# Optimization experiments

Measured on AMD Instinct MI355X. Metric: run time of the kernel, lower is better.

Reference implementation:

```python
import jax, jax.numpy as jnp
import numpy as np

N_HEADS = 16
EPS = 1e-6

def _feature_map(x):
    return jax.nn.elu(x) + 1.0

def setup_inputs() -> dict:
    key = jax.random.key(0)
    k1, k2, k3 = jax.random.split(key, 3)
    B, S, D = 1, 2048, 1024
    x = jax.random.normal(k1, (B, S, D), dtype=jnp.float32)
    causal_mask = jnp.tril(jnp.ones((S, S), dtype=bool))[None, None]  # (1,1,S,S)
    # scale weights like nn.Linear default init (roughly 1/sqrt(fan_in))
    W_qkv = jax.random.normal(k2, (D, 3 * D), dtype=jnp.float32) / np.sqrt(D)
    W_out = jax.random.normal(k3, (D, D), dtype=jnp.float32) / np.sqrt(D)
    return {"x": x, "causal_mask": causal_mask, "W_qkv": W_qkv, "W_out": W_out}

def reference(x, causal_mask, W_qkv, W_out):
    B, S, D = x.shape
    H = N_HEADS
    hd = D // H
    qkv = x @ W_qkv                              # (B,S,3D)
    q, k, v = jnp.split(qkv, 3, axis=-1)
    def to_heads(t):
        return t.reshape(B, S, H, hd).transpose(0, 2, 1, 3)  # (B,H,S,hd)
    q, k, v = to_heads(q), to_heads(k), to_heads(v)
    phi_q = _feature_map(q)
    phi_k = _feature_map(k)
    k_cum = jnp.cumsum(phi_k, axis=2)                        # (B,H,S,hd)
    kv = jnp.einsum('bhsi,bhsj->bhsij', phi_k, v)            # (B,H,S,hd,hd)
    kv_cum = jnp.cumsum(kv, axis=2)
    numer = jnp.einsum('bhsi,bhsij->bhsj', phi_q, kv_cum)    # (B,H,S,hd)
    denom = jnp.einsum('bhsi,bhsi->bhs', phi_q, k_cum) + EPS
    attn_out = numer / denom[..., None]
    attn_out = attn_out.transpose(0, 2, 1, 3).reshape(B, S, D)
    return attn_out @ W_out
```

## Files before the change

### kernel.cpp

```cpp
#include <hip/hip_runtime.h>
#include <cstddef>
#include <cstdint>

#define SEQ 2048
#define DIM 1024
#define NH 16
#define HD 64
#define CK 64
#define NCK (SEQ / CK)
#define KVR 65
#define KVRP 80

typedef __attribute__((ext_vector_type(8))) short short8;
typedef __attribute__((ext_vector_type(8))) unsigned short ushort8;
typedef __attribute__((ext_vector_type(4))) float fx4;

__device__ __forceinline__ float phi_fn(float x) {
    return x > 0.f ? x + 1.f : __expf(x);
}
__device__ __forceinline__ float bf2f(unsigned short u) {
    return __uint_as_float((unsigned int)u << 16);
}
__device__ __forceinline__ unsigned short f2bf(float f) {
    unsigned int u = __float_as_uint(f);
    unsigned int r = (u + 0x7FFFu + ((u >> 16) & 1u)) >> 16;
    return (unsigned short)r;
}

__device__ __forceinline__ short8 lds_read_frag(const unsigned short* base, int row, int kcol) {
    int byte = row * 128 + kcol * 2; byte ^= (row & 7) << 4;
    return *(const short8*)((const char*)base + byte);
}

__device__ __forceinline__ int swz_t(int row, int col) {
    int byte = row * 128 + col * 2;
    return byte ^ ((((row & 7) ^ ((row >> 3) & 7))) << 4);
}
__device__ __forceinline__ void lds_write16_t(unsigned short* base, int row, int col, ushort8 v) {
    *(ushort8*)((char*)base + swz_t(row, col)) = v;
}
__device__ __forceinline__ void lds_write2_t(unsigned short* base, int row, int col, unsigned short v) {
    *(unsigned short*)((char*)base + swz_t(row, col)) = v;
}
__device__ __forceinline__ short8 lds_read_frag_t(const unsigned short* base, int row, int kcol) {
    return *(const short8*)((const char*)base + swz_t(row, kcol));
}

template<int N> __device__ __forceinline__ void waitv() {
    if constexpr (N == 0)      asm volatile("s_waitcnt vmcnt(0)" ::: "memory");
    else if constexpr (N == 3) asm volatile("s_waitcnt vmcnt(3)" ::: "memory");
    else if constexpr (N == 6) asm volatile("s_waitcnt vmcnt(6)" ::: "memory");
    else if constexpr (N == 7) asm volatile("s_waitcnt vmcnt(7)" ::: "memory");
    else                       asm volatile("s_waitcnt vmcnt(0)" ::: "memory");
}

__global__ __launch_bounds__(256)
void prep_fused(const float* __restrict__ x, unsigned short* __restrict__ xb,
                const float* __restrict__ W1, unsigned short* __restrict__ WT1,
                const float* __restrict__ W2, unsigned short* __restrict__ WT2)
{
    __shared__ float t[32][33];
    int b = blockIdx.x;
    if (b < 2048) {
        const int i = (b * 256 + threadIdx.x) * 4;
        float4 v = *(const float4*)&x[i];
        ushort4 o;
        o.x = f2bf(v.x); o.y = f2bf(v.y); o.z = f2bf(v.z); o.w = f2bf(v.w);
        *(ushort4*)&xb[i] = o;
        return;
    }
    b -= 2048;
    const float* W; unsigned short* WT; int N, kb, nb;
    if (b < 96 * 32) {
        W = W1; WT = WT1; N = 3 * DIM;
        nb = (b % 96) * 32; kb = (b / 96) * 32;
    } else {
        b -= 96 * 32;
        W = W2; WT = WT2; N = DIM;
        nb = (b % 32) * 32; kb = (b / 32) * 32;
    }
    const int c = threadIdx.x & 31, r0 = threadIdx.x >> 5;
    #pragma unroll
    for (int i = 0; i < 4; ++i) {
        const int r = r0 + i * 8;
        t[r][c] = W[(size_t)(kb + r) * N + nb + c];
    }
    __syncthreads();
    #pragma unroll
    for (int i = 0; i < 4; ++i) {
        const int r = r0 + i * 8;
        WT[(size_t)(nb + r) * DIM + kb + c] = f2bf(t[c][r]);
    }
}

template<int WAVES_M, int WAVES_N, int NFRAG, int SLOTS_A, int SLOTS_B,
         int MINW, int OUT_BF16, int PHI>
__global__ __launch_bounds__(WAVES_M * WAVES_N * 64, MINW)
void gemm_pipe(const unsigned short* __restrict__ A,
               const unsigned short* __restrict__ BT,
               void* __restrict__ Cout, int M, int N, int K)
{
    constexpr int BN      = WAVES_N * NFRAG * 16;
    constexpr int THREADS = WAVES_M * WAVES_N * 64;
    constexpr int CHUNK   = THREADS * 16;
    constexpr int ALOADS  = (128 * 64 * 2) / CHUNK;
    constexpr int BLOADS  = (BN * 64 * 2) / CHUNK;
    constexpr int WAITN   = (SLOTS_A == 3 ? ALOADS : 0) + (SLOTS_B == 3 ? BLOADS : 0);

    __shared__ unsigned short As[SLOTS_A][128 * 64];
    __shared__ unsigned short Bs[SLOTS_B][BN * 64];

    const int tid = threadIdx.x, lane = tid & 63, wave = tid >> 6;
    const int wm = (wave / WAVES_N) * 64;
    const int wn = (wave % WAVES_N) * (NFRAG * 16);

    int wg = blockIdx.y * gridDim.x + blockIdx.x;
    const int cpx = (gridDim.x * gridDim.y) >> 3;
    wg = (wg & 7) * cpx + (wg >> 3);
    const int bx = wg / gridDim.y;
    const int by = wg % gridDim.y;

    const int m0 = by * 128, n0 = bx * BN;
    const unsigned short* Abase = A + (size_t)m0 * K;
    const unsigned short* Bbase = BT + (size_t)n0 * K;
    const int nt = K >> 6;
    const int fr = lane & 15, fk = (lane >> 4) * 8;

    fx4 acc[4][NFRAG] = {};

    auto STAGE_A = [&](int slot, int t) {
        const int k0 = t << 6;
        #pragma unroll
        for (int q = 0; q < ALOADS; ++q) {
            const int L = q * CHUNK + tid * 16;
            const int row = L >> 7;
            const int srcb = L ^ ((row & 7) << 4);
            const unsigned short* g = Abase + (size_t)row * K + k0 + ((srcb & 127) >> 1);
            __builtin_amdgcn_global_load_lds(
                (const __attribute__((address_space(1))) void*)g,
                (__attribute__((address_space(3))) void*)((char*)&As[slot][0] + q * CHUNK + wave * 1024),
                16, 0, 0);
        }
    };
    auto STAGE_B = [&](int slot, int t) {
        const int k0 = t << 6;
        #pragma unroll
        for (int q = 0; q < BLOADS; ++q) {
            const int L = q * CHUNK + tid * 16;
            const int row = L >> 7;
            const int srcb = L ^ ((row & 7) << 4);
            const unsigned short* g = Bbase + (size_t)row * K + k0 + ((srcb & 127) >> 1);
            __builtin_amdgcn_global_load_lds(
                (const __attribute__((address_space(1))) void*)g,
                (__attribute__((address_space(3))) void*)((char*)&Bs[slot][0] + q * CHUNK + wave * 1024),
                16, 0, 0);
        }
    };

    STAGE_A(0, 0); STAGE_B(0, 0);
    if constexpr (SLOTS_A == 3) STAGE_A(1, 1);
    if constexpr (SLOTS_B == 3) STAGE_B(1, 1);
    waitv<WAITN>();
    __builtin_amdgcn_s_barrier();

    int ca = 0, cb = 0;
    for (int t = 0; t < nt; ++t) {
        short8 a0[4], a1[4], b0[NFRAG], b1[NFRAG];
        #pragma unroll
        for (int i = 0; i < 4; ++i) {
            a0[i] = lds_read_frag(&As[ca][0], wm + i * 16 + fr, fk);
            a1[i] = lds_read_frag(&As[ca][0], wm + i * 16 + fr, 32 + fk);
        }
        #pragma unroll
        for (int j = 0; j < NFRAG; ++j) {
            b0[j] = lds_read_frag(&Bs[cb][0], wn + j * 16 + fr, fk);
            b1[j] = lds_read_frag(&Bs[cb][0], wn + j * 16 + fr, 32 + fk);
        }

        if (t + SLOTS_A - 1 < nt)
            STAGE_A((ca + SLOTS_A - 1) % SLOTS_A, t + SLOTS_A - 1);
        if (t + SLOTS_B - 1 < nt)
            STAGE_B((cb + SLOTS_B - 1) % SLOTS_B, t + SLOTS_B - 1);

        __builtin_amdgcn_s_setprio(1);
        #pragma unroll
        for (int i = 0; i < 4; ++i)
            #pragma unroll
            for (int j = 0; j < NFRAG; ++j)
                acc[i][j] = __builtin_amdgcn_mfma_f32_16x16x32_bf16(a0[i], b0[j], acc[i][j], 0, 0, 0);
        #pragma unroll
        for (int i = 0; i < 4; ++i)
            #pragma unroll
            for (int j = 0; j < NFRAG; ++j)
                acc[i][j] = __builtin_amdgcn_mfma_f32_16x16x32_bf16(a1[i], b1[j], acc[i][j], 0, 0, 0);
        __builtin_amdgcn_s_setprio(0);

        if (t + 2 < nt) waitv<WAITN>(); else waitv<0>();
        __builtin_amdgcn_s_barrier();
        ca = (ca + 1) % SLOTS_A;
        cb = (cb + 1) % SLOTS_B;
    }

    const int cr = (lane >> 4) * 4, cc = lane & 15;
    #pragma unroll
    for (int i = 0; i < 4; ++i)
        #pragma unroll
        for (int j = 0; j < NFRAG; ++j) {
            const int m = m0 + wm + i * 16 + cr;
            const int n = n0 + wn + j * 16 + cc;
            #pragma unroll
            for (int r = 0; r < 4; ++r) {
                float v = acc[i][j][r];
                if (PHI && n < 2 * DIM) v = phi_fn(v);
                if (OUT_BF16)
                    ((unsigned short*)Cout)[(size_t)(m + r) * N + n] = f2bf(v);
                else
                    ((float*)Cout)[(size_t)(m + r) * N + n] = v;
            }
        }
}

__global__ __launch_bounds__(256)
void chunk_kv(const unsigned short* __restrict__ qkv, float* __restrict__ kvs)
{
    const int c = blockIdx.x, h = blockIdx.y;
    __shared__ unsigned short kT[64 * 64];
    __shared__ unsigned short vT[KVRP * 64];
    const int tid = threadIdx.x, lane = tid & 63, wave = tid >> 6;
    const int s0 = c * CK;

    #pragma unroll
    for (int part = 0; part < 2; ++part) {
        const int s = (tid >> 3) + part * 32;
        const int d0 = (tid & 7) * 8;
        const size_t base = (size_t)(s0 + s) * (3 * DIM) + (size_t)h * HD + d0;
        ushort8 kk = *(const ushort8*)&qkv[base + DIM];
        ushort8 vv = *(const ushort8*)&qkv[base + 2 * DIM];
        #pragma unroll
        for (int u = 0; u < 8; ++u) {
            lds_write2_t(kT, d0 + u, s, kk[u]);
            lds_write2_t(vT, d0 + u, s, vv[u]);
        }
    }
    if (tid < 64) lds_write2_t(vT, 64, tid, 0x3F80);
    for (int idx = tid; idx < 15 * 64; idx += 256)
        lds_write2_t(vT, 65 + (idx >> 6), idx & 63, 0);
    __syncthreads();

    fx4 acc[5] = {};
    #pragma unroll
    for (int ks = 0; ks < 2; ++ks) {
        short8 b = lds_read_frag_t(kT, wave * 16 + (lane & 15), ks * 32 + (lane >> 4) * 8);
        #pragma unroll
        for (int mt = 0; mt < 5; ++mt) {
            short8 a = lds_read_frag_t(vT, mt * 16 + (lane & 15), ks * 32 + (lane >> 4) * 8);
            acc[mt] = __builtin_amdgcn_mfma_f32_16x16x32_bf16(a, b, acc[mt], 0, 0, 0);
        }
    }
    float* dst = kvs + (size_t)(h * NCK + c) * KVR * 64;
    const int i = wave * 16 + (lane & 15);
    #pragma unroll
    for (int mt = 0; mt < 5; ++mt)
        #pragma unroll
        for (int t = 0; t < 4; ++t) {
            const int j = mt * 16 + (lane >> 4) * 4 + t;
            if (j < KVR) dst[(size_t)j * 64 + i] = acc[mt][t];
        }
}

__global__ __launch_bounds__(256)
void scan_kv(const float* __restrict__ kvs, unsigned short* __restrict__ kvpb)
{
    const int e = blockIdx.x * 256 + threadIdx.x;
    if (e >= NH * KVR * 64) return;
    const int h = e / (KVR * 64), off = e % (KVR * 64);
    const float* src = kvs + (size_t)h * NCK * KVR * 64 + off;
    unsigned short* dst = kvpb + (size_t)h * NCK * KVR * 64 + off;
    float v[NCK];
    #pragma unroll
    for (int c2 = 0; c2 < NCK; ++c2) v[c2] = src[(size_t)c2 * KVR * 64];
    float run = 0.f;
    #pragma unroll
    for (int c2 = 0; c2 < NCK; ++c2) {
        dst[(size_t)c2 * KVR * 64] = f2bf(run);
        run += v[c2];
    }
}

__global__ __launch_bounds__(256)
void attn_chunk(const unsigned short* __restrict__ qkv,
                const unsigned short* __restrict__ kvpb,
                unsigned short* __restrict__ attnb)
{
    const int c = blockIdx.x, h = blockIdx.y;
    __shared__ unsigned short q_s[64 * 64];
    __shared__ unsigned short k_s[64 * 64];
    __shared__ unsigned short p_s[64 * 64];
    __shared__ unsigned short vT[KVRP * 64];
    __shared__ unsigned short kvp[KVRP * 64];
    const int tid = threadIdx.x, lane = tid & 63, wave = tid >> 6;
    const int s0 = c * CK;

    #pragma unroll
    for (int part = 0; part < 2; ++part) {
        const int s = (tid >> 3) + part * 32;
        const int d0 = (tid & 7) * 8;
        const size_t base = (size_t)(s0 + s) * (3 * DIM) + (size_t)h * HD + d0;
        ushort8 qq = *(const ushort8*)&qkv[base];
        ushort8 kk = *(const ushort8*)&qkv[base + DIM];
        ushort8 vv = *(const ushort8*)&qkv[base + 2 * DIM];
        lds_write16_t(q_s, s, d0, qq);
        lds_write16_t(k_s, s, d0, kk);
        #pragma unroll
        for (int u = 0; u < 8; ++u)
            lds_write2_t(vT, d0 + u, s, vv[u]);
    }
    {
        const unsigned short* kv_src = kvpb + (size_t)(h * NCK + c) * KVR * 64;
        for (int idx = tid * 8; idx < KVR * 64; idx += 2048) {
            ushort8 kv8 = *(const ushort8*)&kv_src[idx];
            lds_write16_t(kvp, idx >> 6, idx & 63, kv8);
        }
    }
    if (tid < 64) lds_write2_t(vT, 64, tid, 0x3F80);
    for (int idx = tid; idx < 15 * 64; idx += 256) {
        lds_write2_t(vT, 65 + (idx >> 6), idx & 63, 0);
        lds_write2_t(kvp, 65 + (idx >> 6), idx & 63, 0);
    }
    __syncthreads();

    const int r0 = wave * 16;
    fx4 accp[4] = {};
    #pragma unroll
    for (int ks = 0; ks < 2; ++ks) {
        short8 aq = lds_read_frag_t(q_s, r0 + (lane & 15), ks * 32 + (lane >> 4) * 8);
        #pragma unroll
        for (int nt = 0; nt < 4; ++nt) {
            short8 bk = lds_read_frag_t(k_s, nt * 16 + (lane & 15), ks * 32 + (lane >> 4) * 8);
            accp[nt] = __builtin_amdgcn_mfma_f32_16x16x32_bf16(aq, bk, accp[nt], 0, 0, 0);
        }
    }
    #pragma unroll
    for (int nt = 0; nt < 4; ++nt)
        #pragma unroll
        for (int t = 0; t < 4; ++t) {
            const int r = r0 + (lane >> 4) * 4 + t, sc = nt * 16 + (lane & 15);
            lds_write2_t(p_s, r, sc, (sc <= r) ? f2bf(accp[nt][t]) : (unsigned short)0);
        }
    __syncthreads();

    fx4 acc[5] = {};
    #pragma unroll
    for (int ks = 0; ks < 2; ++ks) {
        short8 ap = lds_read_frag_t(p_s, r0 + (lane & 15), ks * 32 + (lane >> 4) * 8);
        short8 aq = lds_read_frag_t(q_s, r0 + (lane & 15), ks * 32 + (lane >> 4) * 8);
        #pragma unroll
        for (int nt = 0; nt < 5; ++nt) {
            short8 bv  = lds_read_frag_t(vT,  nt * 16 + (lane & 15), ks * 32 + (lane >> 4) * 8);
            short8 bkv = lds_read_frag_t(kvp, nt * 16 + (lane & 15), ks * 32 + (lane >> 4) * 8);
            acc[nt] = __builtin_amdgcn_mfma_f32_16x16x32_bf16(ap, bv,  acc[nt], 0, 0, 0);
            acc[nt] = __builtin_amdgcn_mfma_f32_16x16x32_bf16(aq, bkv, acc[nt], 0, 0, 0);
        }
    }
    float dinv[4];
    #pragma unroll
    for (int t = 0; t < 4; ++t) {
        const float d = __shfl(acc[4][t], lane & 48, 64);
        dinv[t] = 1.f / (d + 1e-6f);
    }
    #pragma unroll
    for (int nt = 0; nt < 4; ++nt)
        #pragma unroll
        for (int t = 0; t < 4; ++t) {
            const int r = r0 + (lane >> 4) * 4 + t, j = nt * 16 + (lane & 15);
            attnb[(size_t)(s0 + r) * DIM + (size_t)h * HD + j] = f2bf(acc[nt][t] * dinv[t]);
        }
}

extern "C" void kernel_launch(void* const* d_in, const int* in_sizes, int n_in,
                              void* d_out, int out_size, void* d_ws, size_t ws_size,
                              hipStream_t stream)
{
    const float* x     = (const float*)d_in[0];
    const float* W_qkv = (const float*)d_in[2];
    const float* W_out = (const float*)d_in[3];
    float* out = (float*)d_out;

    char* ws = (char*)d_ws;
    size_t off = 0;
    unsigned short* qkvb = (unsigned short*)(ws + off); off += (size_t)SEQ * 3 * DIM * 2;
    unsigned short* xb   = (unsigned short*)(ws + off); off += (size_t)SEQ * DIM * 2;
    float*          kvs  = (float*)         (ws + off); off += (size_t)NH * NCK * KVR * 64 * 4;
    unsigned short* kvpb = (unsigned short*)(ws + off); off += (size_t)NH * NCK * KVR * 64 * 2;
    unsigned short* wqt  = (unsigned short*)(ws + off); off += (size_t)3 * DIM * DIM * 2;
    unsigned short* wot  = (unsigned short*)(ws + off); off += (size_t)DIM * DIM * 2;
    unsigned short* attnb = xb;

    dim3 blk(256);

    prep_fused<<<dim3(2048 + 96 * 32 + 32 * 32), blk, 0, stream>>>(
        x, xb, W_qkv, wqt, W_out, wot);

    gemm_pipe<2, 2, 3, 2, 3, 2, 1, 1><<<dim3(3 * DIM / 96, SEQ / 128), dim3(256), 0, stream>>>(
        xb, wqt, qkvb, SEQ, 3 * DIM, DIM);

    chunk_kv<<<dim3(NCK, NH), blk, 0, stream>>>(qkvb, kvs);
    scan_kv<<<dim3((NH * KVR * 64 + 255) / 256), blk, 0, stream>>>(kvs, kvpb);
    attn_chunk<<<dim3(NCK, NH), blk, 0, stream>>>(qkvb, kvpb, attnb);

    gemm_pipe<2, 2, 2, 3, 3, 2, 0, 0><<<dim3(DIM / 64, SEQ / 128), dim3(256), 0, stream>>>(
        attnb, wot, out, SEQ, DIM, DIM);
}
```

Before: 56.97 us.

## Load QKV GEMM A-operand fragments directly into registers, double-buffered

Adds a gemm_regA kernel for the QKV projection. Each wave reads its A fragments straight from global memory into registers, double-buffered across k-steps, while B still goes through a 3-slot LDS pipeline with global_load_lds. This removes LDS staging and LDS reads for A and frees LDS, at the cost of higher register pressure. A is no longer shared between waves, so the two waves along N each fetch the same A rows, which raises global/L2 traffic. The vmcnt wait counts are retuned for the new load mix.

```diff
diff --git a/kernel.cpp b/kernel.cpp
--- a/kernel.cpp
+++ b/kernel.cpp
@@ -47,11 +47,12 @@
 }
 
 template<int N> __device__ __forceinline__ void waitv() {
-    if constexpr (N == 0)      asm volatile("s_waitcnt vmcnt(0)" ::: "memory");
-    else if constexpr (N == 3) asm volatile("s_waitcnt vmcnt(3)" ::: "memory");
-    else if constexpr (N == 6) asm volatile("s_waitcnt vmcnt(6)" ::: "memory");
-    else if constexpr (N == 7) asm volatile("s_waitcnt vmcnt(7)" ::: "memory");
-    else                       asm volatile("s_waitcnt vmcnt(0)" ::: "memory");
+    if constexpr (N == 0)       asm volatile("s_waitcnt vmcnt(0)"  ::: "memory");
+    else if constexpr (N == 3)  asm volatile("s_waitcnt vmcnt(3)"  ::: "memory");
+    else if constexpr (N == 6)  asm volatile("s_waitcnt vmcnt(6)"  ::: "memory");
+    else if constexpr (N == 8)  asm volatile("s_waitcnt vmcnt(8)"  ::: "memory");
+    else if constexpr (N == 11) asm volatile("s_waitcnt vmcnt(11)" ::: "memory");
+    else                        asm volatile("s_waitcnt vmcnt(0)"  ::: "memory");
 }
 
 __global__ __launch_bounds__(256)
@@ -93,22 +94,18 @@
     }
 }
 
-template<int WAVES_M, int WAVES_N, int NFRAG, int SLOTS_A, int SLOTS_B,
-         int MINW, int OUT_BF16, int PHI>
-__global__ __launch_bounds__(WAVES_M * WAVES_N * 64, MINW)
-void gemm_pipe(const unsigned short* __restrict__ A,
+template<int WAVES_N, int NFRAG, int OUT_BF16, int PHI>
+__global__ __launch_bounds__(WAVES_N * 128, 2)
+void gemm_regA(const unsigned short* __restrict__ A,
                const unsigned short* __restrict__ BT,
                void* __restrict__ Cout, int M, int N, int K)
 {
     constexpr int BN      = WAVES_N * NFRAG * 16;
-    constexpr int THREADS = WAVES_M * WAVES_N * 64;
+    constexpr int THREADS = WAVES_N * 128;
     constexpr int CHUNK   = THREADS * 16;
-    constexpr int ALOADS  = (128 * 64 * 2) / CHUNK;
     constexpr int BLOADS  = (BN * 64 * 2) / CHUNK;
-    constexpr int WAITN   = (SLOTS_A == 3 ? ALOADS : 0) + (SLOTS_B == 3 ? BLOADS : 0);
-
-    __shared__ unsigned short As[SLOTS_A][128 * 64];
-    __shared__ unsigned short Bs[SLOTS_B][BN * 64];
+
+    __shared__ unsigned short Bs[3][BN * 64];
 
     const int tid = threadIdx.x, lane = tid & 63, wave = tid >> 6;
     const int wm = (wave / WAVES_N) * 64;
@@ -121,25 +118,19 @@
     const int by = wg % gridDim.y;
 
     const int m0 = by * 128, n0 = bx * BN;
-    const unsigned short* Abase = A + (size_t)m0 * K;
     const unsigned short* Bbase = BT + (size_t)n0 * K;
     const int nt = K >> 6;
     const int fr = lane & 15, fk = (lane >> 4) * 8;
 
+    const unsigned short* Arow = A + (size_t)(m0 + wm + fr) * K + fk;
+
     fx4 acc[4][NFRAG] = {};
 
-    auto STAGE_A = [&](int slot, int t) {
-        const int k0 = t << 6;
-        #pragma unroll
-        for (int q = 0; q < ALOADS; ++q) {
-            const int L = q * CHUNK + tid * 16;
-            const int row = L >> 7;
-            const int srcb = L ^ ((row & 7) << 4);
-            const unsigned short* g = Abase + (size_t)row * K + k0 + ((srcb & 127) >> 1);
-            __builtin_amdgcn_global_load_lds(
-                (const __attribute__((address_space(1))) void*)g,
-                (__attribute__((address_space(3))) void*)((char*)&As[slot][0] + q * CHUNK + wave * 1024),
-                16, 0, 0);
+    auto LOADA = [&](short8* dst, int t) {
+        #pragma unroll
+        for (int i = 0; i < 4; ++i) {
+            dst[2 * i]     = *(const short8*)(Arow + (size_t)i * 16 * K + t * 64);
+            dst[2 * i + 1] = *(const short8*)(Arow + (size_t)i * 16 * K + t * 64 + 32);
         }
     };
     auto STAGE_B = [&](int slot, int t) {
@@ -157,48 +148,46 @@
         }
     };
 
-    STAGE_A(0, 0); STAGE_B(0, 0);
-    if constexpr (SLOTS_A == 3) STAGE_A(1, 1);
-    if constexpr (SLOTS_B == 3) STAGE_B(1, 1);
-    waitv<WAITN>();
-    __builtin_amdgcn_s_barrier();
-
-    int ca = 0, cb = 0;
-    for (int t = 0; t < nt; ++t) {
-        short8 a0[4], a1[4], b0[NFRAG], b1[NFRAG];
-        #pragma unroll
-        for (int i = 0; i < 4; ++i) {
-            a0[i] = lds_read_frag(&As[ca][0], wm + i * 16 + fr, fk);
-            a1[i] = lds_read_frag(&As[ca][0], wm + i * 16 + fr, 32 + fk);
-        }
+    short8 aE[8], aO[8];
+
+    auto STEP = [&](int t, short8* cur, short8* nxt) {
+        if (t + 1 < nt) LOADA(nxt, t + 1);
+        const int cb = t % 3;
+        short8 b0[NFRAG], b1[NFRAG];
         #pragma unroll
         for (int j = 0; j < NFRAG; ++j) {
             b0[j] = lds_read_frag(&Bs[cb][0], wn + j * 16 + fr, fk);
             b1[j] = lds_read_frag(&Bs[cb][0], wn + j * 16 + fr, 32 + fk);
         }
-
-        if (t + SLOTS_A - 1 < nt)
-            STAGE_A((ca + SLOTS_A - 1) % SLOTS_A, t + SLOTS_A - 1);
-        if (t + SLOTS_B - 1 < nt)
-            STAGE_B((cb + SLOTS_B - 1) % SLOTS_B, t + SLOTS_B - 1);
+        if (t + 2 < nt) STAGE_B((t + 2) % 3, t + 2);
 
         __builtin_amdgcn_s_setprio(1);
         #pragma unroll
         for (int i = 0; i < 4; ++i)
             #pragma unroll
             for (int j = 0; j < NFRAG; ++j)
-                acc[i][j] = __builtin_amdgcn_mfma_f32_16x16x32_bf16(a0[i], b0[j], acc[i][j], 0, 0, 0);
+                acc[i][j] = __builtin_amdgcn_mfma_f32_16x16x32_bf16(cur[2 * i], b0[j], acc[i][j], 0, 0, 0);
         #pragma unroll
         for (int i = 0; i < 4; ++i)
             #pragma unroll
             for (int j = 0; j < NFRAG; ++j)
-                acc[i][j] = __builtin_amdgcn_mfma_f32_16x16x32_bf16(a1[i], b1[j], acc[i][j], 0, 0, 0);
+                acc[i][j] = __builtin_amdgcn_mfma_f32_16x16x32_bf16(cur[2 * i + 1], b1[j], acc[i][j], 0, 0, 0);
         __builtin_amdgcn_s_setprio(0);
 
-        if (t + 2 < nt) waitv<WAITN>(); else waitv<0>();
+        if (t + 2 < nt)      waitv<11>();
+        else if (t + 1 < nt) waitv<8>();
+        else                 waitv<0>();
         __builtin_amdgcn_s_barrier();
-        ca = (ca + 1) % SLOTS_A;
-        cb = (cb + 1) % SLOTS_B;
+    };
+
+    STAGE_B(0, 0); STAGE_B(1, 1);
+    LOADA(aE, 0);
+    waitv<11>();
+    __builtin_amdgcn_s_barrier();
+
+    for (int t = 0; t < nt; t += 2) {
+        STEP(t,     aE, aO);
+        STEP(t + 1, aO, aE);
     }
 
     const int cr = (lane >> 4) * 4, cc = lane & 15;
@@ -220,6 +209,133 @@
         }
 }
 
+template<int WAVES_M, int WAVES_N, int NFRAG, int SLOTS_A, int SLOTS_B,
+         int MINW, int OUT_BF16, int PHI>
+__global__ __launch_bounds__(WAVES_M * WAVES_N * 64, MINW)
+void gemm_pipe(const unsigned short* __restrict__ A,
+               const unsigned short* __restrict__ BT,
+               void* __restrict__ Cout, int M, int N, int K)
+{
+    constexpr int BN      = WAVES_N * NFRAG * 16;
+    constexpr int THREADS = WAVES_M * WAVES_N * 64;
+    constexpr int CHUNK   = THREADS * 16;
+    constexpr int ALOADS  = (128 * 64 * 2) / CHUNK;
+    constexpr int BLOADS  = (BN * 64 * 2) / CHUNK;
+    constexpr int WAITN   = (SLOTS_A == 3 ? ALOADS : 0) + (SLOTS_B == 3 ? BLOADS : 0);
+
+    __shared__ unsigned short As[SLOTS_A][128 * 64];
+    __shared__ unsigned short Bs[SLOTS_B][BN * 64];
+
+    const int tid = threadIdx.x, lane = tid & 63, wave = tid >> 6;
+    const int wm = (wave / WAVES_N) * 64;
+    const int wn = (wave % WAVES_N) * (NFRAG * 16);
+
+    int wg = blockIdx.y * gridDim.x + blockIdx.x;
+    const int cpx = (gridDim.x * gridDim.y) >> 3;
+    wg = (wg & 7) * cpx + (wg >> 3);
+    const int bx = wg / gridDim.y;
+    const int by = wg % gridDim.y;
+
+    const int m0 = by * 128, n0 = bx * BN;
+    const unsigned short* Abase = A + (size_t)m0 * K;
+    const unsigned short* Bbase = BT + (size_t)n0 * K;
+    const int nt = K >> 6;
+    const int fr = lane & 15, fk = (lane >> 4) * 8;
+
+    fx4 acc[4][NFRAG] = {};
+
+    auto STAGE_A = [&](int slot, int t) {
+        const int k0 = t << 6;
+        #pragma unroll
+        for (int q = 0; q < ALOADS; ++q) {
+            const int L = q * CHUNK + tid * 16;
+            const int row = L >> 7;
+            const int srcb = L ^ ((row & 7) << 4);
+            const unsigned short* g = Abase + (size_t)row * K + k0 + ((srcb & 127) >> 1);
+            __builtin_amdgcn_global_load_lds(
+                (const __attribute__((address_space(1))) void*)g,
+                (__attribute__((address_space(3))) void*)((char*)&As[slot][0] + q * CHUNK + wave * 1024),
+                16, 0, 0);
+        }
+    };
+    auto STAGE_B = [&](int slot, int t) {
+        const int k0 = t << 6;
+        #pragma unroll
+        for (int q = 0; q < BLOADS; ++q) {
+            const int L = q * CHUNK + tid * 16;
+            const int row = L >> 7;
+            const int srcb = L ^ ((row & 7) << 4);
+            const unsigned short* g = Bbase + (size_t)row * K + k0 + ((srcb & 127) >> 1);
+            __builtin_amdgcn_global_load_lds(
+                (const __attribute__((address_space(1))) void*)g,
+                (__attribute__((address_space(3))) void*)((char*)&Bs[slot][0] + q * CHUNK + wave * 1024),
+                16, 0, 0);
+        }
+    };
+
+    STAGE_A(0, 0); STAGE_B(0, 0);
+    if constexpr (SLOTS_A == 3) STAGE_A(1, 1);
+    if constexpr (SLOTS_B == 3) STAGE_B(1, 1);
+    waitv<WAITN>();
+    __builtin_amdgcn_s_barrier();
+
+    int ca = 0, cb = 0;
+    for (int t = 0; t < nt; ++t) {
+        short8 a0[4], a1[4], b0[NFRAG], b1[NFRAG];
+        #pragma unroll
+        for (int i = 0; i < 4; ++i) {
+            a0[i] = lds_read_frag(&As[ca][0], wm + i * 16 + fr, fk);
+            a1[i] = lds_read_frag(&As[ca][0], wm + i * 16 + fr, 32 + fk);
+        }
+        #pragma unroll
+        for (int j = 0; j < NFRAG; ++j) {
+            b0[j] = lds_read_frag(&Bs[cb][0], wn + j * 16 + fr, fk);
+            b1[j] = lds_read_frag(&Bs[cb][0], wn + j * 16 + fr, 32 + fk);
+        }
+
+        if (t + SLOTS_A - 1 < nt)
+            STAGE_A((ca + SLOTS_A - 1) % SLOTS_A, t + SLOTS_A - 1);
+        if (t + SLOTS_B - 1 < nt)
+            STAGE_B((cb + SLOTS_B - 1) % SLOTS_B, t + SLOTS_B - 1);
+
+        __builtin_amdgcn_s_setprio(1);
+        #pragma unroll
+        for (int i = 0; i < 4; ++i)
+            #pragma unroll
+            for (int j = 0; j < NFRAG; ++j)
+                acc[i][j] = __builtin_amdgcn_mfma_f32_16x16x32_bf16(a0[i], b0[j], acc[i][j], 0, 0, 0);
+        #pragma unroll
+        for (int i = 0; i < 4; ++i)
+            #pragma unroll
+            for (int j = 0; j < NFRAG; ++j)
+                acc[i][j] = __builtin_amdgcn_mfma_f32_16x16x32_bf16(a1[i], b1[j], acc[i][j], 0, 0, 0);
+        __builtin_amdgcn_s_setprio(0);
+
+        if (t + 2 < nt) waitv<WAITN>(); else waitv<0>();
+        __builtin_amdgcn_s_barrier();
+        ca = (ca + 1) % SLOTS_A;
+        cb = (cb + 1) % SLOTS_B;
+    }
+
+    const int cr = (lane >> 4) * 4, cc = lane & 15;
+    #pragma unroll
+    for (int i = 0; i < 4; ++i)
+        #pragma unroll
+        for (int j = 0; j < NFRAG; ++j) {
+            const int m = m0 + wm + i * 16 + cr;
+            const int n = n0 + wn + j * 16 + cc;
+            #pragma unroll
+            for (int r = 0; r < 4; ++r) {
+                float v = acc[i][j][r];
+                if (PHI && n < 2 * DIM) v = phi_fn(v);
+                if (OUT_BF16)
+                    ((unsigned short*)Cout)[(size_t)(m + r) * N + n] = f2bf(v);
+                else
+                    ((float*)Cout)[(size_t)(m + r) * N + n] = v;
+            }
+        }
+}
+
 __global__ __launch_bounds__(256)
 void chunk_kv(const unsigned short* __restrict__ qkv, float* __restrict__ kvs)
 {
@@ -401,7 +517,7 @@
     prep_fused<<<dim3(2048 + 96 * 32 + 32 * 32), blk, 0, stream>>>(
         x, xb, W_qkv, wqt, W_out, wot);
 
-    gemm_pipe<2, 2, 3, 2, 3, 2, 1, 1><<<dim3(3 * DIM / 96, SEQ / 128), dim3(256), 0, stream>>>(
+    gemm_regA<2, 3, 1, 1><<<dim3(3 * DIM / 96, SEQ / 128), dim3(256), 0, stream>>>(
         xb, wqt, qkvb, SEQ, 3 * DIM, DIM);
 
     chunk_kv<<<dim3(NCK, NH), blk, 0, stream>>>(qkvb, kvs);
```

After: 76.95 us. 35.1% more time.
